# Kernel optimization log

Measured on AMD Instinct MI355X. Metric: run time of the kernel, lower is better.

## Reference

```python
import jax, jax.numpy as jnp
import numpy as np

B, C, H, W, T = 2, 96, 64, 64, 64
NH = 8  # num_heads
WS = 2  # window size per axis (2,2,2)


def setup_inputs() -> dict:
    key = jax.random.key(0)
    ks = jax.random.split(key, 9)
    s = lambda fan_in: 1.0 / np.sqrt(fan_in)
    return {
        "x": jax.random.normal(ks[0], (B, C, H, W, T), dtype=jnp.float32),
        # linear weights stored [in, out] (transposed vs torch nn.Linear)
        "qkv_w": jax.random.normal(ks[1], (C, 3 * C), dtype=jnp.float32) * s(C),
        "qkv_b": jax.random.normal(ks[2], (3 * C,), dtype=jnp.float32) * 0.01,
        "merge_w": jax.random.normal(ks[3], (C, C), dtype=jnp.float32) * s(C),
        "merge_b": jax.random.normal(ks[4], (C,), dtype=jnp.float32) * 0.01,
        "w1": jax.random.normal(ks[5], (2 * C, C), dtype=jnp.float32) * s(2 * C),
        "b1": jax.random.normal(ks[6], (C,), dtype=jnp.float32) * 0.01,
        "w2": jax.random.normal(ks[7], (C, C), dtype=jnp.float32) * s(C),
        "b2": jax.random.normal(ks[8], (C,), dtype=jnp.float32) * 0.01,
    }


def reference(x, qkv_w, qkv_b, merge_w, merge_b, w1, b1, w2, b2):
    b, c, h, w, t = x.shape
    hd = c // NH
    scale = hd ** -0.5
    n = WS * WS * WS  # 8 tokens per window

    xp = jnp.transpose(x, (0, 2, 3, 4, 1))  # [B,H,W,T,C]
    # window partition -> [B*nWin, 8, C]
    xw = xp.reshape(b, h // WS, WS, w // WS, WS, t // WS, WS, c)
    xw = jnp.transpose(xw, (0, 1, 3, 5, 2, 4, 6, 7)).reshape(-1, n, c)

    # windowed MHSA
    qkv = (xw @ qkv_w + qkv_b).reshape(-1, n, 3, NH, hd)
    q, k, v = jnp.moveaxis(qkv, 2, 0)  # each [Bw, n, NH, hd]
    attn = jax.nn.softmax(jnp.einsum('bnhd,bmhd->bhnm', q * scale, k), axis=-1)
    msg = jnp.einsum('bhnm,bmhd->bnhd', attn, v).reshape(-1, n, c)
    msg = msg @ merge_w + merge_b

    # window reverse -> [B,H,W,T,C]
    msg = msg.reshape(b, h // WS, w // WS, t // WS, WS, WS, WS, c)
    msg = jnp.transpose(msg, (0, 1, 4, 2, 5, 3, 6, 7)).reshape(b, h, w, t, c)

    # concat residual path + MLP (GELU exact, matching torch nn.GELU default)
    xt = xp.reshape(b, h * w * t, c)
    mt = msg.reshape(b, h * w * t, c)
    hmid = jax.nn.gelu(jnp.concatenate([xt, mt], axis=-1) @ w1 + b1, approximate=False)
    out = hmid @ w2 + b2
    return jnp.transpose(out.reshape(b, h, w, t, c), (0, 4, 1, 2, 3))
```

## Files before the change

### kernel.cpp

```cpp
#include <hip/hip_runtime.h>
#include <math.h>

typedef short bf16x8 __attribute__((ext_vector_type(8)));
typedef float f32x4 __attribute__((ext_vector_type(4)));

__device__ __forceinline__ ushort f2bf(float f) {
  union { float f; unsigned int i; } v; v.f = f;
  unsigned int x = v.i;
  return (ushort)((x + 0x7fffu + ((x >> 16) & 1u)) >> 16);
}
__device__ __forceinline__ float bf2f(ushort u) {
  union { unsigned int i; float f; } v; v.i = ((unsigned int)u) << 16; return v.f;
}

__device__ __forceinline__ void cp16(const ushort* g, ushort* l) {
  __builtin_amdgcn_global_load_lds(
      (const __attribute__((address_space(1))) void*)g,
      (__attribute__((address_space(3))) void*)l, 16, 0, 0);
}
__device__ __forceinline__ void stage_chunk(const ushort* __restrict__ g,
                                            ushort* l, int tid) {
  for (int i = tid; i < 1152; i += 256) cp16(g + i * 8, l + i * 8);
}

__global__ void swizzle_w(const float* __restrict__ qkv_w,
                          const float* __restrict__ merge_w,
                          const float* __restrict__ w1,
                          const float* __restrict__ w2,
                          ushort* __restrict__ ws) {
  int g = blockIdx.x * 256 + threadIdx.x;
  if (g >= 8064) return;
  int tile = g >> 6, lane = g & 63;
  const float* src; int ld, c0, k0, rem;
  if (tile < 54)       { rem = tile % 18; src = qkv_w;   ld = 288; c0 = (tile / 18) * 96 + (rem / 3) * 16; k0 = (rem % 3) * 32; }
  else if (tile < 72)  { rem = tile - 54; src = merge_w; ld = 96;  c0 = (rem / 3) * 16; k0 = (rem % 3) * 32; }
  else if (tile < 90)  { rem = tile - 72; src = w1;      ld = 96;  c0 = (rem / 3) * 16; k0 = (rem % 3) * 32; }
  else if (tile < 108) { rem = tile - 90; src = w1;      ld = 96;  c0 = (rem / 3) * 16; k0 = 96 + (rem % 3) * 32; }
  else                 { rem = tile - 108; src = w2;     ld = 96;  c0 = (rem / 3) * 16; k0 = (rem % 3) * 32; }
  int n = c0 + (lane & 15);
  int kb = k0 + (lane >> 4) * 8;
  ushort tmp[8];
#pragma unroll
  for (int j = 0; j < 8; ++j) tmp[j] = f2bf(src[(size_t)(kb + j) * ld + n]);
  *(uint4*)(ws + tile * 512 + lane * 8) = *(const uint4*)tmp;
}

#define KPAD 104
#define QPAD 66
#define OPAD 65
__global__ __launch_bounds__(256, 2) void swin_mfma(
    const float* __restrict__ x,
    const float* __restrict__ qkv_b, const float* __restrict__ merge_b,
    const float* __restrict__ b1, const float* __restrict__ b2,
    const ushort* __restrict__ wsw, float* __restrict__ out) {
  __shared__ __align__(16) ushort Xs[64 * KPAD];
  __shared__ __align__(16) ushort R[19008];
  __shared__ __align__(16) ushort Ws[9216];

  const int tid = threadIdx.x, bid = blockIdx.x;
  const int t0 = bid & 3, w0 = (bid >> 2) & 31, h0 = (bid >> 7) & 31, b = bid >> 12;
  const int lane = tid & 63, wave = tid >> 6;
  const int mrow = lane & 15, quad = lane >> 4;
  const int arow = (wave * 16 + mrow) * KPAD + quad * 8;
  const int tokb = wave * 16 + quad * 4;

  for (int i = tid; i < 1536; i += 256) {
    int q = i & 3, dw = (i >> 2) & 1, dh = (i >> 3) & 1, c = i >> 4;
    size_t g = ((((size_t)b * 96 + c) * 64 + h0 * 2 + dh) * 64 + w0 * 2 + dw) * 64 + t0 * 16 + q * 4;
    float4 v = *(const float4*)(x + g);
    float vv[4] = {v.x, v.y, v.z, v.w};
    int base = dh * 4 + dw * 2;
#pragma unroll
    for (int j = 0; j < 4; ++j) {
      int tl = q * 4 + j;
      Xs[((tl >> 1) * 8 + base + (tl & 1)) * KPAD + c] = f2bf(vv[j]);
    }
  }
  stage_chunk(wsw + 0 * 9216, Ws, tid);
  __syncthreads();

  bf16x8 aX[3];
#pragma unroll
  for (int kt = 0; kt < 3; ++kt)
    aX[kt] = *(const bf16x8*)(Xs + arow + kt * 32);

  for (int cn = 0; cn < 3; ++cn) {
    __syncthreads();
#pragma unroll
    for (int nt = 0; nt < 6; ++nt) {
      int col = cn * 96 + nt * 16 + mrow;
      float bias = qkv_b[col];
      f32x4 acc = {bias, bias, bias, bias};
#pragma unroll
      for (int kt = 0; kt < 3; ++kt) {
        bf16x8 bf = *(const bf16x8*)(Ws + (nt * 3 + kt) * 512 + lane * 8);
        acc = __builtin_amdgcn_mfma_f32_16x16x32_bf16(aX[kt], bf, acc, 0, 0, 0);
      }
#pragma unroll
      for (int r = 0; r < 4; ++r) R[col * QPAD + tokb + r] = f2bf(acc[r]);
    }
    __syncthreads();
    if (cn < 2) stage_chunk(wsw + (cn + 1) * 9216, Ws, tid);
  }

  {
    const int win = tid >> 5, head = (tid >> 2) & 7, r2 = (tid & 3) * 2;
    const ushort* Qb = R + (head * 12) * QPAD + win * 8;
    const ushort* Kb = R + (96 + head * 12) * QPAD + win * 8;
    const ushort* Vb = R + (192 + head * 12) * QPAD + win * 8;
    const float scale = 0.28867513459481287f;
    float q0[12], q1[12];
#pragma unroll
    for (int d = 0; d < 12; ++d) { q0[d] = bf2f(Qb[d * QPAD + r2]); q1[d] = bf2f(Qb[d * QPAD + r2 + 1]); }
    float s0[8], s1[8];
#pragma unroll
    for (int m = 0; m < 8; ++m) {
      float a0 = 0.f, a1 = 0.f;
#pragma unroll
      for (int d = 0; d < 12; ++d) {
        float kv = bf2f(Kb[d * QPAD + m]);
        a0 += q0[d] * kv; a1 += q1[d] * kv;
      }
      s0[m] = a0 * scale; s1[m] = a1 * scale;
    }
    float mx0 = s0[0], mx1 = s1[0];
#pragma unroll
    for (int m = 1; m < 8; ++m) { mx0 = fmaxf(mx0, s0[m]); mx1 = fmaxf(mx1, s1[m]); }
    float sum0 = 0.f, sum1 = 0.f;
#pragma unroll
    for (int m = 0; m < 8; ++m) {
      s0[m] = __expf(s0[m] - mx0); sum0 += s0[m];
      s1[m] = __expf(s1[m] - mx1); sum1 += s1[m];
    }
    float inv0 = 1.0f / sum0, inv1 = 1.0f / sum1;
    float o0[12] = {}, o1[12] = {};
#pragma unroll
    for (int m = 0; m < 8; ++m) {
      float p0 = s0[m] * inv0, p1 = s1[m] * inv1;
#pragma unroll
      for (int d = 0; d < 12; ++d) {
        float vv = bf2f(Vb[d * QPAD + m]);
        o0[d] += p0 * vv; o1[d] += p1 * vv;
      }
    }
    __syncthreads();
    int tr = win * 8 + r2;
#pragma unroll
    for (int d = 0; d < 12; ++d) {
      R[tr * KPAD + head * 12 + d] = f2bf(o0[d]);
      R[(tr + 1) * KPAD + head * 12 + d] = f2bf(o1[d]);
    }
  }
  stage_chunk(wsw + 3 * 9216, Ws, tid);
  __syncthreads();

  {
    bf16x8 aM[3];
#pragma unroll
    for (int kt = 0; kt < 3; ++kt) aM[kt] = *(const bf16x8*)(R + arow + kt * 32);
#pragma unroll
    for (int nt = 0; nt < 6; ++nt) {
      int col = nt * 16 + mrow;
      float bias = merge_b[col];
      f32x4 acc = {bias, bias, bias, bias};
#pragma unroll
      for (int kt = 0; kt < 3; ++kt) {
        bf16x8 bf = *(const bf16x8*)(Ws + (nt * 3 + kt) * 512 + lane * 8);
        acc = __builtin_amdgcn_mfma_f32_16x16x32_bf16(aM[kt], bf, acc, 0, 0, 0);
      }
#pragma unroll
      for (int r = 0; r < 4; ++r) R[(tokb + r) * KPAD + col] = f2bf(acc[r]);
    }
  }
  __syncthreads();
  stage_chunk(wsw + 4 * 9216, Ws, tid);
  __syncthreads();

  {
    bf16x8 aX2[3];
#pragma unroll
    for (int kt = 0; kt < 3; ++kt) aX2[kt] = *(const bf16x8*)(Xs + arow + kt * 32);
    f32x4 accH[6];
#pragma unroll
    for (int nt = 0; nt < 6; ++nt) {
      int col = nt * 16 + mrow;
      float bias = b1[col];
      f32x4 acc = {bias, bias, bias, bias};
#pragma unroll
      for (int kt = 0; kt < 3; ++kt) {
        bf16x8 bf = *(const bf16x8*)(Ws + (nt * 3 + kt) * 512 + lane * 8);
        acc = __builtin_amdgcn_mfma_f32_16x16x32_bf16(aX2[kt], bf, acc, 0, 0, 0);
      }
      accH[nt] = acc;
    }
    __syncthreads();
    stage_chunk(wsw + 5 * 9216, Ws, tid);
    bf16x8 aM2[3];
#pragma unroll
    for (int kt = 0; kt < 3; ++kt) aM2[kt] = *(const bf16x8*)(R + arow + kt * 32);
    __syncthreads();
#pragma unroll
    for (int nt = 0; nt < 6; ++nt) {
      f32x4 acc = accH[nt];
#pragma unroll
      for (int kt = 0; kt < 3; ++kt) {
        bf16x8 bf = *(const bf16x8*)(Ws + (nt * 3 + kt) * 512 + lane * 8);
        acc = __builtin_amdgcn_mfma_f32_16x16x32_bf16(aM2[kt], bf, acc, 0, 0, 0);
      }
      int col = nt * 16 + mrow;
#pragma unroll
      for (int r = 0; r < 4; ++r) {
        float h = acc[r];
        float gel = 0.5f * h * (1.0f + erff(h * 0.70710678118654752f));
        R[6656 + (tokb + r) * KPAD + col] = f2bf(gel);
      }
    }
  }
  __syncthreads();
  stage_chunk(wsw + 6 * 9216, Ws, tid);
  __syncthreads();

  {
    bf16x8 aH[3];
#pragma unroll
    for (int kt = 0; kt < 3; ++kt) aH[kt] = *(const bf16x8*)(R + 6656 + arow + kt * 32);
#pragma unroll
    for (int nt = 0; nt < 6; ++nt) {
      int col = nt * 16 + mrow;
      float bias = b2[col];
      f32x4 acc = {bias, bias, bias, bias};
#pragma unroll
      for (int kt = 0; kt < 3; ++kt) {
        bf16x8 bf = *(const bf16x8*)(Ws + (nt * 3 + kt) * 512 + lane * 8);
        acc = __builtin_amdgcn_mfma_f32_16x16x32_bf16(aH[kt], bf, acc, 0, 0, 0);
      }
#pragma unroll
      for (int r = 0; r < 4; ++r) R[col * OPAD + tokb + r] = f2bf(acc[r]);
    }
  }
  __syncthreads();

  for (int i = tid; i < 1536; i += 256) {
    int q = i & 3, dw = (i >> 2) & 1, dh = (i >> 3) & 1, c = i >> 4;
    float vv[4];
#pragma unroll
    for (int j = 0; j < 4; ++j) {
      int tl = q * 4 + j;
      vv[j] = bf2f(R[c * OPAD + (tl >> 1) * 8 + dh * 4 + dw * 2 + (tl & 1)]);
    }
    float4 v = {vv[0], vv[1], vv[2], vv[3]};
    size_t g = ((((size_t)b * 96 + c) * 64 + h0 * 2 + dh) * 64 + w0 * 2 + dw) * 64 + t0 * 16 + q * 4;
    *(float4*)(out + g) = v;
  }
}

extern "C" void kernel_launch(void* const* d_in, const int* in_sizes, int n_in,
                              void* d_out, int out_size, void* d_ws, size_t ws_size,
                              hipStream_t stream) {
  const float* x = (const float*)d_in[0];
  const float* qkv_w = (const float*)d_in[1];
  const float* qkv_b = (const float*)d_in[2];
  const float* merge_w = (const float*)d_in[3];
  const float* merge_b = (const float*)d_in[4];
  const float* w1 = (const float*)d_in[5];
  const float* b1 = (const float*)d_in[6];
  const float* w2 = (const float*)d_in[7];
  const float* b2 = (const float*)d_in[8];
  ushort* wsw = (ushort*)d_ws;
  swizzle_w<<<dim3(32), dim3(256), 0, stream>>>(qkv_w, merge_w, w1, w2, wsw);
  swin_mfma<<<dim3(8192), dim3(256), 0, stream>>>(
      x, qkv_b, merge_b, b1, b2, wsw, (float*)d_out);
}
```

Before: 620.0 us.

## Read swizzled weights directly from global memory instead of staging through LDS

Removes the shared-memory weight buffer and the global_load_lds staging steps, so each MFMA B-fragment is loaded straight from the pre-swizzled bf16 weight array in global memory (expected to hit in L2 or cache). This drops the 18 KB Ws buffer and several __syncthreads barriers, and merges the two halves of the w1 GEMM into one loop. Lower LDS use may allow more resident blocks per CU. The cost is repeated global or L2 loads of weights by every wave, adding memory latency inside the MFMA loops.

```diff
diff --git a/kernel.cpp b/kernel.cpp
--- a/kernel.cpp
+++ b/kernel.cpp
@@ -11,16 +11,6 @@
 }
 __device__ __forceinline__ float bf2f(ushort u) {
   union { unsigned int i; float f; } v; v.i = ((unsigned int)u) << 16; return v.f;
-}
-
-__device__ __forceinline__ void cp16(const ushort* g, ushort* l) {
-  __builtin_amdgcn_global_load_lds(
-      (const __attribute__((address_space(1))) void*)g,
-      (__attribute__((address_space(3))) void*)l, 16, 0, 0);
-}
-__device__ __forceinline__ void stage_chunk(const ushort* __restrict__ g,
-                                            ushort* l, int tid) {
-  for (int i = tid; i < 1152; i += 256) cp16(g + i * 8, l + i * 8);
 }
 
 __global__ void swizzle_w(const float* __restrict__ qkv_w,
@@ -55,7 +45,6 @@
     const ushort* __restrict__ wsw, float* __restrict__ out) {
   __shared__ __align__(16) ushort Xs[64 * KPAD];
   __shared__ __align__(16) ushort R[19008];
-  __shared__ __align__(16) ushort Ws[9216];
 
   const int tid = threadIdx.x, bid = blockIdx.x;
   const int t0 = bid & 3, w0 = (bid >> 2) & 31, h0 = (bid >> 7) & 31, b = bid >> 12;
@@ -76,7 +65,6 @@
       Xs[((tl >> 1) * 8 + base + (tl & 1)) * KPAD + c] = f2bf(vv[j]);
     }
   }
-  stage_chunk(wsw + 0 * 9216, Ws, tid);
   __syncthreads();
 
   bf16x8 aX[3];
@@ -85,7 +73,6 @@
     aX[kt] = *(const bf16x8*)(Xs + arow + kt * 32);
 
   for (int cn = 0; cn < 3; ++cn) {
-    __syncthreads();
 #pragma unroll
     for (int nt = 0; nt < 6; ++nt) {
       int col = cn * 96 + nt * 16 + mrow;
@@ -93,15 +80,14 @@
       f32x4 acc = {bias, bias, bias, bias};
 #pragma unroll
       for (int kt = 0; kt < 3; ++kt) {
-        bf16x8 bf = *(const bf16x8*)(Ws + (nt * 3 + kt) * 512 + lane * 8);
+        bf16x8 bf = *(const bf16x8*)(wsw + (size_t)(cn * 18 + nt * 3 + kt) * 512 + lane * 8);
         acc = __builtin_amdgcn_mfma_f32_16x16x32_bf16(aX[kt], bf, acc, 0, 0, 0);
       }
 #pragma unroll
       for (int r = 0; r < 4; ++r) R[col * QPAD + tokb + r] = f2bf(acc[r]);
     }
-    __syncthreads();
-    if (cn < 2) stage_chunk(wsw + (cn + 1) * 9216, Ws, tid);
-  }
+  }
+  __syncthreads();
 
   {
     const int win = tid >> 5, head = (tid >> 2) & 7, r2 = (tid & 3) * 2;
@@ -151,7 +137,6 @@
       R[(tr + 1) * KPAD + head * 12 + d] = f2bf(o1[d]);
     }
   }
-  stage_chunk(wsw + 3 * 9216, Ws, tid);
   __syncthreads();
 
   {
@@ -165,7 +150,7 @@
       f32x4 acc = {bias, bias, bias, bias};
 #pragma unroll
       for (int kt = 0; kt < 3; ++kt) {
-        bf16x8 bf = *(const bf16x8*)(Ws + (nt * 3 + kt) * 512 + lane * 8);
+        bf16x8 bf = *(const bf16x8*)(wsw + (size_t)(54 + nt * 3 + kt) * 512 + lane * 8);
         acc = __builtin_amdgcn_mfma_f32_16x16x32_bf16(aM[kt], bf, acc, 0, 0, 0);
       }
 #pragma unroll
@@ -173,14 +158,14 @@
     }
   }
   __syncthreads();
-  stage_chunk(wsw + 4 * 9216, Ws, tid);
-  __syncthreads();
-
-  {
-    bf16x8 aX2[3];
-#pragma unroll
-    for (int kt = 0; kt < 3; ++kt) aX2[kt] = *(const bf16x8*)(Xs + arow + kt * 32);
-    f32x4 accH[6];
+
+  {
+    bf16x8 aX2[3], aM2[3];
+#pragma unroll
+    for (int kt = 0; kt < 3; ++kt) {
+      aX2[kt] = *(const bf16x8*)(Xs + arow + kt * 32);
+      aM2[kt] = *(const bf16x8*)(R + arow + kt * 32);
+    }
 #pragma unroll
     for (int nt = 0; nt < 6; ++nt) {
       int col = nt * 16 + mrow;
@@ -188,26 +173,14 @@
       f32x4 acc = {bias, bias, bias, bias};
 #pragma unroll
       for (int kt = 0; kt < 3; ++kt) {
-        bf16x8 bf = *(const bf16x8*)(Ws + (nt * 3 + kt) * 512 + lane * 8);
+        bf16x8 bf = *(const bf16x8*)(wsw + (size_t)(72 + nt * 3 + kt) * 512 + lane * 8);
         acc = __builtin_amdgcn_mfma_f32_16x16x32_bf16(aX2[kt], bf, acc, 0, 0, 0);
       }
-      accH[nt] = acc;
-    }
-    __syncthreads();
-    stage_chunk(wsw + 5 * 9216, Ws, tid);
-    bf16x8 aM2[3];
-#pragma unroll
-    for (int kt = 0; kt < 3; ++kt) aM2[kt] = *(const bf16x8*)(R + arow + kt * 32);
-    __syncthreads();
-#pragma unroll
-    for (int nt = 0; nt < 6; ++nt) {
-      f32x4 acc = accH[nt];
-#pragma unroll
-      for (int kt = 0; kt < 3; ++kt) {
-        bf16x8 bf = *(const bf16x8*)(Ws + (nt * 3 + kt) * 512 + lane * 8);
+#pragma unroll
+      for (int kt = 0; kt < 3; ++kt) {
+        bf16x8 bf = *(const bf16x8*)(wsw + (size_t)(90 + nt * 3 + kt) * 512 + lane * 8);
         acc = __builtin_amdgcn_mfma_f32_16x16x32_bf16(aM2[kt], bf, acc, 0, 0, 0);
       }
-      int col = nt * 16 + mrow;
 #pragma unroll
       for (int r = 0; r < 4; ++r) {
         float h = acc[r];
@@ -217,8 +190,6 @@
     }
   }
   __syncthreads();
-  stage_chunk(wsw + 6 * 9216, Ws, tid);
-  __syncthreads();
 
   {
     bf16x8 aH[3];
@@ -231,7 +202,7 @@
       f32x4 acc = {bias, bias, bias, bias};
 #pragma unroll
       for (int kt = 0; kt < 3; ++kt) {
-        bf16x8 bf = *(const bf16x8*)(Ws + (nt * 3 + kt) * 512 + lane * 8);
+        bf16x8 bf = *(const bf16x8*)(wsw + (size_t)(108 + nt * 3 + kt) * 512 + lane * 8);
         acc = __builtin_amdgcn_mfma_f32_16x16x32_bf16(aH[kt], bf, acc, 0, 0, 0);
       }
 #pragma unroll
```

New measurement: 559.1 us. 9.8% less time.
